# Performance work log

Hardware: AMD Instinct MI355X
Metric: run time of the kernel (lower is better)

## Reference

```python
import jax, jax.numpy as jnp
import numpy as np

N_HEAD = 12
N_TILES = 10  # forward hardcodes t = T // 10 and repeats the tril mask 10x10


def setup_inputs() -> dict:
    key = jax.random.key(0)
    ks = jax.random.split(key, 9)
    B, T, C = 2, 2560, 768
    s = 1.0 / np.sqrt(C)
    x = jax.random.normal(ks[0], (B, T, C), dtype=jnp.float32)
    Wk = jax.random.normal(ks[1], (C, C), dtype=jnp.float32) * s
    bk = jnp.zeros((C,), dtype=jnp.float32)
    Wq = jax.random.normal(ks[2], (C, C), dtype=jnp.float32) * s
    bq = jnp.zeros((C,), dtype=jnp.float32)
    Wv = jax.random.normal(ks[3], (C, C), dtype=jnp.float32) * s
    bv = jnp.zeros((C,), dtype=jnp.float32)
    Wp = jax.random.normal(ks[4], (C, C), dtype=jnp.float32) * s
    bp = jnp.zeros((C,), dtype=jnp.float32)
    return {"x": x, "Wk": Wk, "bk": bk, "Wq": Wq, "bq": bq,
            "Wv": Wv, "bv": bv, "Wp": Wp, "bp": bp}


def reference(x, Wk, bk, Wq, bq, Wv, bv, Wp, bp):
    B, T, C = x.shape
    hd = C // N_HEAD
    t = T // N_TILES
    # linear projections (torch nn.Linear: x @ W.T + b)
    k = (x @ Wk.T + bk).reshape(B, T, N_HEAD, hd).transpose(0, 2, 1, 3)  # [B,H,T,hd]
    q = (x @ Wq.T + bq).reshape(B, T, N_HEAD, hd).transpose(0, 2, 1, 3)
    v = (x @ Wv.T + bv).reshape(B, T, N_HEAD, hd).transpose(0, 2, 1, 3)
    att = jnp.einsum('bhqd,bhkd->bhqk', q, k) * (1.0 / np.sqrt(hd))  # [B,H,T,T]
    # repeated block-tril mask: tril(t,t) tiled 10x10 over TxT
    idx = jnp.arange(T)
    mask = (idx[:, None] % t) >= (idx[None, :] % t)  # [T,T] bool
    att = jnp.where(mask[None, None], att, -jnp.inf)
    att = jax.nn.softmax(att, axis=-1)
    y = jnp.einsum('bhqk,bhkd->bhqd', att, v)  # [B,H,T,hd]
    y = y.transpose(0, 2, 1, 3).reshape(B, T, C)
    return y @ Wp.T + bp
```

## Files before the change

### kernel.cpp

```cpp
#include <hip/hip_runtime.h>

typedef unsigned short u16;
typedef unsigned int u32;
typedef __bf16 bf16x8 __attribute__((ext_vector_type(8)));
typedef short s16x4 __attribute__((ext_vector_type(4)));
typedef float f32x4 __attribute__((ext_vector_type(4)));

#define CC 768
#define TT 2560
#define NH 12
#define HD 64
#define KDIM 768

#define QSCALE 0.18033688011112042f

__device__ __forceinline__ u16 f2bf(float f) {
  u32 u = __builtin_bit_cast(u32, f);
  u32 r = u + 0x7fffu + ((u >> 16) & 1u);
  return (u16)(r >> 16);
}

#if __has_builtin(__builtin_amdgcn_mfma_f32_16x16x16bf16_1k)
__device__ __forceinline__ f32x4 mfma16b(s16x4 a, s16x4 b, f32x4 c) {
  return __builtin_amdgcn_mfma_f32_16x16x16bf16_1k(a, b, c, 0, 0, 0);
}
#else
__device__ __forceinline__ f32x4 mfma16b(s16x4 a, s16x4 b, f32x4 c) {
  f32x4 d;
  asm("v_mfma_f32_16x16x16_bf16 %0, %1, %2, %3\n\ts_nop 7\n\ts_nop 7"
      : "=v"(d) : "v"(a), "v"(b), "v"(c));
  return d;
}
#endif

__global__ void convall(const float* __restrict__ x,
                        const float* __restrict__ Wq, const float* __restrict__ Wk,
                        const float* __restrict__ Wv, const float* __restrict__ Wp,
                        u16* __restrict__ xb, u16* __restrict__ wqb, u16* __restrict__ wkb,
                        u16* __restrict__ wvb, u16* __restrict__ wpb,
                        int nx4, int nw4) {
  int z = blockIdx.y;
  const float* in; u16* out; int n4;
  switch (z) {
    case 0: in = x;  out = xb;  n4 = nx4; break;
    case 1: in = Wq; out = wqb; n4 = nw4; break;
    case 2: in = Wk; out = wkb; n4 = nw4; break;
    case 3: in = Wv; out = wvb; n4 = nw4; break;
    default: in = Wp; out = wpb; n4 = nw4; break;
  }
  int i = blockIdx.x * blockDim.x + threadIdx.x;
  if (i >= n4) return;
  float4 v = ((const float4*)in)[i];
  ushort4 o;
  o.x = f2bf(v.x); o.y = f2bf(v.y); o.z = f2bf(v.z); o.w = f2bf(v.w);
  ((ushort4*)out)[i] = o;
}

__global__ __launch_bounds__(256) void gemm_qkv(
    const u16* __restrict__ xb,
    const u16* __restrict__ wqb, const u16* __restrict__ wkb, const u16* __restrict__ wvb,
    const float* __restrict__ bq, const float* __restrict__ bk, const float* __restrict__ bv,
    u16* __restrict__ qo, u16* __restrict__ ko, u16* __restrict__ vo)
{
  __shared__ __align__(16) u16 lds_a[128 * 72];
  __shared__ __align__(16) u16 lds_b[128 * 72];
  int z = blockIdx.z;
  const u16* W = (z == 0) ? wqb : (z == 1 ? wkb : wvb);
  const float* bias = (z == 0) ? bq : (z == 1 ? bk : bv);
  int n0 = blockIdx.x * 128;
  int m0 = blockIdx.y * 128;
  int tid = threadIdx.x;
  int lane = tid & 63, wv_ = tid >> 6;
  int wm = wv_ & 1, wn = wv_ >> 1;
  int mcol = lane & 15, quad = lane >> 4;
  int chunk = tid & 7, rbase = tid >> 3;

  f32x4 acc[4][4] = {};

  for (int k0 = 0; k0 < KDIM; k0 += 64) {
    __syncthreads();
#pragma unroll
    for (int r = 0; r < 4; ++r) {
      int row = rbase + r * 32;
      *(uint4*)&lds_a[row * 72 + chunk * 8] =
          *(const uint4*)&xb[(size_t)(m0 + row) * KDIM + k0 + chunk * 8];
      *(uint4*)&lds_b[row * 72 + chunk * 8] =
          *(const uint4*)&W[(size_t)(n0 + row) * KDIM + k0 + chunk * 8];
    }
    __syncthreads();
#pragma unroll
    for (int kc = 0; kc < 2; ++kc) {
      bf16x8 af[4], bfr[4];
#pragma unroll
      for (int i = 0; i < 4; i++)
        af[i] = *(const bf16x8*)&lds_a[(wm * 64 + i * 16 + mcol) * 72 + kc * 32 + quad * 8];
#pragma unroll
      for (int i = 0; i < 4; i++)
        bfr[i] = *(const bf16x8*)&lds_b[(wn * 64 + i * 16 + mcol) * 72 + kc * 32 + quad * 8];
      if (z == 2) {
#pragma unroll
        for (int i = 0; i < 4; i++)
#pragma unroll
          for (int j = 0; j < 4; j++)
            acc[i][j] = __builtin_amdgcn_mfma_f32_16x16x32_bf16(af[i], bfr[j], acc[i][j], 0, 0, 0);
      } else {
#pragma unroll
        for (int i = 0; i < 4; i++)
#pragma unroll
          for (int j = 0; j < 4; j++)
            acc[i][j] = __builtin_amdgcn_mfma_f32_16x16x32_bf16(bfr[j], af[i], acc[i][j], 0, 0, 0);
      }
    }
  }

  if (z == 2) {
#pragma unroll
    for (int i = 0; i < 4; i++) {
      int rowb = m0 + wm * 64 + i * 16 + quad * 4;
      int b = rowb / TT;
      int tt0 = rowb - b * TT;
#pragma unroll
      for (int j = 0; j < 4; j++) {
        int col = n0 + wn * 64 + j * 16 + mcol;
        int h = col >> 6, d = col & 63;
        float bb_ = bias[col];
        size_t bhoff = (size_t)(b * NH + h) * (TT * HD);
        ushort4 pk;
        pk.x = f2bf(acc[i][j][0] + bb_);
        pk.y = f2bf(acc[i][j][1] + bb_);
        pk.z = f2bf(acc[i][j][2] + bb_);
        pk.w = f2bf(acc[i][j][3] + bb_);
        *(ushort4*)&vo[bhoff + (size_t)(tt0 >> 4) * 1024 + d * 16 + (tt0 & 15)] = pk;
      }
    }
  } else {
    u16* dst = (z == 0) ? qo : ko;
    float scale = (z == 0) ? QSCALE : 1.0f;
#pragma unroll
    for (int i = 0; i < 4; i++) {
      int token = m0 + wm * 64 + i * 16 + mcol;
      int b = token / TT;
      int tt = token - b * TT;
#pragma unroll
      for (int j = 0; j < 4; j++) {
        int ch0 = n0 + wn * 64 + j * 16 + quad * 4;
        int h = ch0 >> 6, d4 = ch0 & 63;
        float4 bb4 = *(const float4*)&bias[ch0];
        size_t bhoff = (size_t)(b * NH + h) * (TT * HD);
        ushort4 pk;
        pk.x = f2bf((acc[i][j][0] + bb4.x) * scale);
        pk.y = f2bf((acc[i][j][1] + bb4.y) * scale);
        pk.z = f2bf((acc[i][j][2] + bb4.z) * scale);
        pk.w = f2bf((acc[i][j][3] + bb4.w) * scale);
        if (z == 0) {
          *(ushort4*)&dst[bhoff + (size_t)tt * HD + d4] = pk;
        } else {
          *(ushort4*)&dst[bhoff + (size_t)(tt >> 4) * 1024 + (d4 >> 5) * 512 +
                          (tt & 15) * 32 + (d4 & 31)] = pk;
        }
      }
    }
  }
}

struct Strip {
  bf16x8 qf0, qf1;
  f32x4 o0, o1, o2, o3;
  f32x4 racc;
};

__device__ __forceinline__ void strip_step(
    Strip& S, bf16x8 kf0, bf16x8 kf1,
    s16x4 vf0, s16x4 vf1, s16x4 vf2, s16x4 vf3,
    bool maskg, int mcol, int quad)
{
  f32x4 st = {0.f, 0.f, 0.f, 0.f};
  st = __builtin_amdgcn_mfma_f32_16x16x32_bf16(kf0, S.qf0, st, 0, 0, 0);
  st = __builtin_amdgcn_mfma_f32_16x16x32_bf16(kf1, S.qf1, st, 0, 0, 0);
  float p0 = __builtin_amdgcn_exp2f(st[0]);
  float p1 = __builtin_amdgcn_exp2f(st[1]);
  float p2 = __builtin_amdgcn_exp2f(st[2]);
  float p3 = __builtin_amdgcn_exp2f(st[3]);
  if (maskg) {
    int j0 = quad * 4;
    p0 = (j0 + 0 > mcol) ? 0.f : p0;
    p1 = (j0 + 1 > mcol) ? 0.f : p1;
    p2 = (j0 + 2 > mcol) ? 0.f : p2;
    p3 = (j0 + 3 > mcol) ? 0.f : p3;
  }
  uint2 pk;
  pk.x = __builtin_amdgcn_perm(__builtin_bit_cast(u32, p1),
                               __builtin_bit_cast(u32, p0), 0x07060302u);
  pk.y = __builtin_amdgcn_perm(__builtin_bit_cast(u32, p3),
                               __builtin_bit_cast(u32, p2), 0x07060302u);
  s16x4 pf = __builtin_bit_cast(s16x4, pk);
  const s16x4 ones = {0x3F80, 0x3F80, 0x3F80, 0x3F80};
  S.racc = mfma16b(ones, pf, S.racc);
  S.o0 = mfma16b(vf0, pf, S.o0);
  S.o1 = mfma16b(vf1, pf, S.o1);
  S.o2 = mfma16b(vf2, pf, S.o2);
  S.o3 = mfma16b(vf3, pf, S.o3);
}

#define OSTR 68

__global__ __launch_bounds__(128) void attn(
    const u16* __restrict__ q, const u16* __restrict__ kg,
    const u16* __restrict__ vg, u16* __restrict__ y)
{
  __shared__ float lds_o[4][16 * OSTR];
  __shared__ float lds_r[64];

  int tid = threadIdx.x;
  int lane = tid & 63, w = tid >> 6;
  int mcol = lane & 15, quad = lane >> 4;
  int gid = blockIdx.x;
  int c = gid & 7;
  int idx = gid >> 3;
  int sub = idx / 40;
  int s = idx - sub * 40;
  int bh = c * 3 + sub;
  int hb = s >> 3;
  int r = s & 7;
  int b = bh / NH, h = bh - b * NH;
  const u16* qp = q + (size_t)bh * TT * HD;
  const u16* kp = kg + (size_t)bh * TT * HD;
  const u16* vp = vg + (size_t)bh * TT * HD;

  int base = hb * 512;
  int rh = 7 - r;
  int qr[4];
  qr[0] = base + r * 16;
  qr[1] = base + 128 + rh * 16;
  qr[2] = base + 256 + r * 16;
  qr[3] = base + 384 + rh * 16;

  Strip S[4];
#pragma unroll
  for (int i = 0; i < 4; ++i) {
    S[i].qf0 = *(const bf16x8*)&qp[(size_t)(qr[i] + mcol) * HD + quad * 8];
    S[i].qf1 = *(const bf16x8*)&qp[(size_t)(qr[i] + mcol) * HD + 32 + quad * 8];
    S[i].o0 = {0.f, 0.f, 0.f, 0.f};
    S[i].o1 = {0.f, 0.f, 0.f, 0.f};
    S[i].o2 = {0.f, 0.f, 0.f, 0.f};
    S[i].o3 = {0.f, 0.f, 0.f, 0.f};
    S[i].racc = {0.f, 0.f, 0.f, 0.f};
  }

  int koff = mcol * 32 + quad * 8;
  int voff = mcol * 16 + quad * 4;

  for (int kt = w * 10; kt < w * 10 + 10; ++kt) {
    const u16* ktb = kp + kt * (128 * HD);
    const u16* vtb = vp + kt * (128 * HD);
    if ((kt & 1) == 0) {
#pragma unroll
      for (int g = 0; g < 8; ++g) {
        bf16x8 kf0 = *(const bf16x8*)&ktb[g * 1024 + koff];
        bf16x8 kf1 = *(const bf16x8*)&ktb[g * 1024 + 512 + koff];
        s16x4 vf0 = *(const s16x4*)&vtb[g * 1024 + 0 * 256 + voff];
        s16x4 vf1 = *(const s16x4*)&vtb[g * 1024 + 1 * 256 + voff];
        s16x4 vf2 = *(const s16x4*)&vtb[g * 1024 + 2 * 256 + voff];
        s16x4 vf3 = *(const s16x4*)&vtb[g * 1024 + 3 * 256 + voff];
        strip_step(S[1], kf0, kf1, vf0, vf1, vf2, vf3, false, mcol, quad);
        strip_step(S[3], kf0, kf1, vf0, vf1, vf2, vf3, false, mcol, quad);
        if (g <= r) {
          bool mg = (g == r);
          strip_step(S[0], kf0, kf1, vf0, vf1, vf2, vf3, mg, mcol, quad);
          strip_step(S[2], kf0, kf1, vf0, vf1, vf2, vf3, mg, mcol, quad);
        }
      }
    } else {
      for (int g = 0; g <= rh; ++g) {
        bf16x8 kf0 = *(const bf16x8*)&ktb[g * 1024 + koff];
        bf16x8 kf1 = *(const bf16x8*)&ktb[g * 1024 + 512 + koff];
        s16x4 vf0 = *(const s16x4*)&vtb[g * 1024 + 0 * 256 + voff];
        s16x4 vf1 = *(const s16x4*)&vtb[g * 1024 + 1 * 256 + voff];
        s16x4 vf2 = *(const s16x4*)&vtb[g * 1024 + 2 * 256 + voff];
        s16x4 vf3 = *(const s16x4*)&vtb[g * 1024 + 3 * 256 + voff];
        bool mg = (g == rh);
        strip_step(S[1], kf0, kf1, vf0, vf1, vf2, vf3, mg, mcol, quad);
        strip_step(S[3], kf0, kf1, vf0, vf1, vf2, vf3, mg, mcol, quad);
      }
    }
  }

  if (w == 1) {
#pragma unroll
    for (int i = 0; i < 4; ++i) {
      f32x4 oo[4] = {S[i].o0, S[i].o1, S[i].o2, S[i].o3};
#pragma unroll
      for (int df = 0; df < 4; ++df)
        *(f32x4*)&lds_o[i][mcol * OSTR + df * 16 + quad * 4] = oo[df];
      if (quad == 0) lds_r[i * 16 + mcol] = S[i].racc[0];
    }
  }
  __syncthreads();
  if (w == 0) {
#pragma unroll
    for (int i = 0; i < 4; ++i) {
      float denom = S[i].racc[0] + lds_r[i * 16 + mcol];
      float inv = 1.0f / denom;
      f32x4 oo[4] = {S[i].o0, S[i].o1, S[i].o2, S[i].o3};
      size_t yrow = ((size_t)(b * TT + qr[i] + mcol)) * CC + h * HD;
#pragma unroll
      for (int df = 0; df < 4; ++df) {
        f32x4 other = *(const f32x4*)&lds_o[i][mcol * OSTR + df * 16 + quad * 4];
        ushort4 pk;
        pk.x = f2bf((oo[df][0] + other[0]) * inv);
        pk.y = f2bf((oo[df][1] + other[1]) * inv);
        pk.z = f2bf((oo[df][2] + other[2]) * inv);
        pk.w = f2bf((oo[df][3] + other[3]) * inv);
        *(ushort4*)&y[yrow + df * 16 + quad * 4] = pk;
      }
    }
  }
}

__global__ __launch_bounds__(256) void gemm_out(
    const u16* __restrict__ yb, const u16* __restrict__ wpb,
    const float* __restrict__ bp, float* __restrict__ out)
{
  __shared__ __align__(16) u16 lds_a[64 * 72];
  __shared__ __align__(16) u16 lds_b[128 * 72];
  int n0 = blockIdx.x * 128;
  int m0 = blockIdx.y * 64;
  int tid = threadIdx.x;
  int lane = tid & 63, wv_ = tid >> 6;
  int wm = wv_ & 1, wn = wv_ >> 1;
  int mcol = lane & 15, quad = lane >> 4;
  int chunk = tid & 7, rbase = tid >> 3;

  f32x4 acc[2][4] = {};

  for (int k0 = 0; k0 < KDIM; k0 += 64) {
    __syncthreads();
#pragma unroll
    for (int r = 0; r < 2; ++r) {
      int row = rbase + r * 32;
      *(uint4*)&lds_a[row * 72 + chunk * 8] =
          *(const uint4*)&yb[(size_t)(m0 + row) * KDIM + k0 + chunk * 8];
    }
#pragma unroll
    for (int r = 0; r < 4; ++r) {
      int row = rbase + r * 32;
      *(uint4*)&lds_b[row * 72 + chunk * 8] =
          *(const uint4*)&wpb[(size_t)(n0 + row) * KDIM + k0 + chunk * 8];
    }
    __syncthreads();
#pragma unroll
    for (int kc = 0; kc < 2; ++kc) {
      bf16x8 af[2], bfr[4];
#pragma unroll
      for (int i = 0; i < 2; i++)
        af[i] = *(const bf16x8*)&lds_a[(wm * 32 + i * 16 + mcol) * 72 + kc * 32 + quad * 8];
#pragma unroll
      for (int j = 0; j < 4; j++)
        bfr[j] = *(const bf16x8*)&lds_b[(wn * 64 + j * 16 + mcol) * 72 + kc * 32 + quad * 8];
#pragma unroll
      for (int i = 0; i < 2; i++)
#pragma unroll
        for (int j = 0; j < 4; j++)
          acc[i][j] = __builtin_amdgcn_mfma_f32_16x16x32_bf16(bfr[j], af[i], acc[i][j], 0, 0, 0);
    }
  }

#pragma unroll
  for (int i = 0; i < 2; i++) {
    int token = m0 + wm * 32 + i * 16 + mcol;
#pragma unroll
    for (int j = 0; j < 4; j++) {
      int ch0 = n0 + wn * 64 + j * 16 + quad * 4;
      float4 bb4 = *(const float4*)&bp[ch0];
      float4 o4;
      o4.x = acc[i][j][0] + bb4.x;
      o4.y = acc[i][j][1] + bb4.y;
      o4.z = acc[i][j][2] + bb4.z;
      o4.w = acc[i][j][3] + bb4.w;
      *(float4*)&out[(size_t)token * CC + ch0] = o4;
    }
  }
}

extern "C" void kernel_launch(void* const* d_in, const int* in_sizes, int n_in,
                              void* d_out, int out_size, void* d_ws, size_t ws_size,
                              hipStream_t stream) {
  const float* x  = (const float*)d_in[0];
  const float* Wk = (const float*)d_in[1];
  const float* bk = (const float*)d_in[2];
  const float* Wq = (const float*)d_in[3];
  const float* bq = (const float*)d_in[4];
  const float* Wv = (const float*)d_in[5];
  const float* bv = (const float*)d_in[6];
  const float* Wp = (const float*)d_in[7];
  const float* bp = (const float*)d_in[8];
  float* out = (float*)d_out;

  char* ws = (char*)d_ws;
  size_t off = 0;
  auto alloc = [&](size_t bytes) {
    void* p = ws + off;
    off += (bytes + 255) & ~(size_t)255;
    return p;
  };
  const size_t NX = (size_t)2 * TT * CC;
  const size_t NW = (size_t)CC * CC;
  u16* xb  = (u16*)alloc(NX * 2);
  u16* wqb = (u16*)alloc(NW * 2);
  u16* wkb = (u16*)alloc(NW * 2);
  u16* wvb = (u16*)alloc(NW * 2);
  u16* wpb = (u16*)alloc(NW * 2);
  u16* qws = (u16*)alloc(NX * 2);
  u16* kws = (u16*)alloc(NX * 2);
  u16* vgw = (u16*)alloc(NX * 2);
  u16* yws = (u16*)alloc(NX * 2);

  int nx4 = (int)(NX / 4), nw4 = (int)(NW / 4);
  convall<<<dim3((nx4 + 255) / 256, 5), 256, 0, stream>>>(
      x, Wq, Wk, Wv, Wp, xb, wqb, wkb, wvb, wpb, nx4, nw4);

  gemm_qkv<<<dim3(6, 40, 3), 256, 0, stream>>>(xb, wqb, wkb, wvb, bq, bk, bv,
                                               qws, kws, vgw);
  attn<<<dim3(960), 128, 0, stream>>>(qws, kws, vgw, yws);
  gemm_out<<<dim3(6, 80), 256, 0, stream>>>(yws, wpb, bp, out);
}
```

Before: 188.8 us.

## Fuse Q/K/V projections into one block sharing the x tile

The QKV GEMM no longer runs a separate grid slice per projection. Each block now computes a 64x64 output tile for all three of Q, K and V at once, loading the x tile into LDS once and reusing it against three weight tiles. This cuts redundant x loads and raises the block count from 720 to 960. In exchange each block does less MFMA work per LDS fragment load, because the per-wave tiles shrink to 32x32 per matrix, and more weight traffic is issued per block.

```diff
diff --git a/kernel.cpp b/kernel.cpp
--- a/kernel.cpp
+++ b/kernel.cpp
@@ -62,103 +62,107 @@
     const float* __restrict__ bq, const float* __restrict__ bk, const float* __restrict__ bv,
     u16* __restrict__ qo, u16* __restrict__ ko, u16* __restrict__ vo)
 {
-  __shared__ __align__(16) u16 lds_a[128 * 72];
-  __shared__ __align__(16) u16 lds_b[128 * 72];
-  int z = blockIdx.z;
-  const u16* W = (z == 0) ? wqb : (z == 1 ? wkb : wvb);
-  const float* bias = (z == 0) ? bq : (z == 1 ? bk : bv);
-  int n0 = blockIdx.x * 128;
-  int m0 = blockIdx.y * 128;
+  __shared__ __align__(16) u16 lds_a[64 * 72];
+  __shared__ __align__(16) u16 lds_b[3][64 * 72];
+  int n0 = blockIdx.x * 64;
+  int m0 = blockIdx.y * 64;
   int tid = threadIdx.x;
   int lane = tid & 63, wv_ = tid >> 6;
   int wm = wv_ & 1, wn = wv_ >> 1;
   int mcol = lane & 15, quad = lane >> 4;
   int chunk = tid & 7, rbase = tid >> 3;
 
-  f32x4 acc[4][4] = {};
+  const u16* Ws0 = wqb; const u16* Ws1 = wkb; const u16* Ws2 = wvb;
+
+  f32x4 acc[3][2][2] = {};
 
   for (int k0 = 0; k0 < KDIM; k0 += 64) {
     __syncthreads();
 #pragma unroll
-    for (int r = 0; r < 4; ++r) {
+    for (int r = 0; r < 2; ++r) {
       int row = rbase + r * 32;
       *(uint4*)&lds_a[row * 72 + chunk * 8] =
           *(const uint4*)&xb[(size_t)(m0 + row) * KDIM + k0 + chunk * 8];
-      *(uint4*)&lds_b[row * 72 + chunk * 8] =
-          *(const uint4*)&W[(size_t)(n0 + row) * KDIM + k0 + chunk * 8];
+      *(uint4*)&lds_b[0][row * 72 + chunk * 8] =
+          *(const uint4*)&Ws0[(size_t)(n0 + row) * KDIM + k0 + chunk * 8];
+      *(uint4*)&lds_b[1][row * 72 + chunk * 8] =
+          *(const uint4*)&Ws1[(size_t)(n0 + row) * KDIM + k0 + chunk * 8];
+      *(uint4*)&lds_b[2][row * 72 + chunk * 8] =
+          *(const uint4*)&Ws2[(size_t)(n0 + row) * KDIM + k0 + chunk * 8];
     }
     __syncthreads();
 #pragma unroll
     for (int kc = 0; kc < 2; ++kc) {
-      bf16x8 af[4], bfr[4];
-#pragma unroll
-      for (int i = 0; i < 4; i++)
-        af[i] = *(const bf16x8*)&lds_a[(wm * 64 + i * 16 + mcol) * 72 + kc * 32 + quad * 8];
-#pragma unroll
-      for (int i = 0; i < 4; i++)
-        bfr[i] = *(const bf16x8*)&lds_b[(wn * 64 + i * 16 + mcol) * 72 + kc * 32 + quad * 8];
-      if (z == 2) {
-#pragma unroll
-        for (int i = 0; i < 4; i++)
-#pragma unroll
-          for (int j = 0; j < 4; j++)
-            acc[i][j] = __builtin_amdgcn_mfma_f32_16x16x32_bf16(af[i], bfr[j], acc[i][j], 0, 0, 0);
-      } else {
-#pragma unroll
-        for (int i = 0; i < 4; i++)
-#pragma unroll
-          for (int j = 0; j < 4; j++)
-            acc[i][j] = __builtin_amdgcn_mfma_f32_16x16x32_bf16(bfr[j], af[i], acc[i][j], 0, 0, 0);
-      }
-    }
-  }
-
-  if (z == 2) {
-#pragma unroll
-    for (int i = 0; i < 4; i++) {
-      int rowb = m0 + wm * 64 + i * 16 + quad * 4;
-      int b = rowb / TT;
-      int tt0 = rowb - b * TT;
-#pragma unroll
-      for (int j = 0; j < 4; j++) {
-        int col = n0 + wn * 64 + j * 16 + mcol;
-        int h = col >> 6, d = col & 63;
-        float bb_ = bias[col];
-        size_t bhoff = (size_t)(b * NH + h) * (TT * HD);
-        ushort4 pk;
-        pk.x = f2bf(acc[i][j][0] + bb_);
-        pk.y = f2bf(acc[i][j][1] + bb_);
-        pk.z = f2bf(acc[i][j][2] + bb_);
-        pk.w = f2bf(acc[i][j][3] + bb_);
-        *(ushort4*)&vo[bhoff + (size_t)(tt0 >> 4) * 1024 + d * 16 + (tt0 & 15)] = pk;
-      }
-    }
-  } else {
-    u16* dst = (z == 0) ? qo : ko;
-    float scale = (z == 0) ? QSCALE : 1.0f;
-#pragma unroll
-    for (int i = 0; i < 4; i++) {
-      int token = m0 + wm * 64 + i * 16 + mcol;
-      int b = token / TT;
-      int tt = token - b * TT;
-#pragma unroll
-      for (int j = 0; j < 4; j++) {
-        int ch0 = n0 + wn * 64 + j * 16 + quad * 4;
-        int h = ch0 >> 6, d4 = ch0 & 63;
-        float4 bb4 = *(const float4*)&bias[ch0];
-        size_t bhoff = (size_t)(b * NH + h) * (TT * HD);
-        ushort4 pk;
-        pk.x = f2bf((acc[i][j][0] + bb4.x) * scale);
-        pk.y = f2bf((acc[i][j][1] + bb4.y) * scale);
-        pk.z = f2bf((acc[i][j][2] + bb4.z) * scale);
-        pk.w = f2bf((acc[i][j][3] + bb4.w) * scale);
-        if (z == 0) {
-          *(ushort4*)&dst[bhoff + (size_t)tt * HD + d4] = pk;
+      bf16x8 af[2];
+#pragma unroll
+      for (int i = 0; i < 2; i++)
+        af[i] = *(const bf16x8*)&lds_a[(wm * 32 + i * 16 + mcol) * 72 + kc * 32 + quad * 8];
+#pragma unroll
+      for (int z = 0; z < 3; ++z) {
+        bf16x8 bfr[2];
+#pragma unroll
+        for (int j = 0; j < 2; j++)
+          bfr[j] = *(const bf16x8*)&lds_b[z][(wn * 32 + j * 16 + mcol) * 72 + kc * 32 + quad * 8];
+        if (z == 2) {
+#pragma unroll
+          for (int i = 0; i < 2; i++)
+#pragma unroll
+            for (int j = 0; j < 2; j++)
+              acc[z][i][j] = __builtin_amdgcn_mfma_f32_16x16x32_bf16(af[i], bfr[j], acc[z][i][j], 0, 0, 0);
         } else {
-          *(ushort4*)&dst[bhoff + (size_t)(tt >> 4) * 1024 + (d4 >> 5) * 512 +
-                          (tt & 15) * 32 + (d4 & 31)] = pk;
+#pragma unroll
+          for (int i = 0; i < 2; i++)
+#pragma unroll
+            for (int j = 0; j < 2; j++)
+              acc[z][i][j] = __builtin_amdgcn_mfma_f32_16x16x32_bf16(bfr[j], af[i], acc[z][i][j], 0, 0, 0);
         }
       }
+    }
+  }
+
+#pragma unroll
+  for (int i = 0; i < 2; i++) {
+    int token = m0 + wm * 32 + i * 16 + mcol;
+    int b = token / TT;
+    int tt = token - b * TT;
+#pragma unroll
+    for (int j = 0; j < 2; j++) {
+      int ch0 = n0 + wn * 32 + j * 16 + quad * 4;
+      int h = ch0 >> 6, d4 = ch0 & 63;
+      size_t bhoff = (size_t)(b * NH + h) * (TT * HD);
+      float4 bq4 = *(const float4*)&bq[ch0];
+      float4 bk4 = *(const float4*)&bk[ch0];
+      ushort4 pq, pk_;
+      pq.x = f2bf((acc[0][i][j][0] + bq4.x) * QSCALE);
+      pq.y = f2bf((acc[0][i][j][1] + bq4.y) * QSCALE);
+      pq.z = f2bf((acc[0][i][j][2] + bq4.z) * QSCALE);
+      pq.w = f2bf((acc[0][i][j][3] + bq4.w) * QSCALE);
+      *(ushort4*)&qo[bhoff + (size_t)tt * HD + d4] = pq;
+      pk_.x = f2bf(acc[1][i][j][0] + bk4.x);
+      pk_.y = f2bf(acc[1][i][j][1] + bk4.y);
+      pk_.z = f2bf(acc[1][i][j][2] + bk4.z);
+      pk_.w = f2bf(acc[1][i][j][3] + bk4.w);
+      *(ushort4*)&ko[bhoff + (size_t)(tt >> 4) * 1024 + (d4 >> 5) * 512 +
+                     (tt & 15) * 32 + (d4 & 31)] = pk_;
+    }
+  }
+#pragma unroll
+  for (int i = 0; i < 2; i++) {
+    int rowb = m0 + wm * 32 + i * 16 + quad * 4;
+    int b = rowb / TT;
+    int tt0 = rowb - b * TT;
+#pragma unroll
+    for (int j = 0; j < 2; j++) {
+      int col = n0 + wn * 32 + j * 16 + mcol;
+      int h = col >> 6, d = col & 63;
+      float bb_ = bv[col];
+      size_t bhoff = (size_t)(b * NH + h) * (TT * HD);
+      ushort4 pk;
+      pk.x = f2bf(acc[2][i][j][0] + bb_);
+      pk.y = f2bf(acc[2][i][j][1] + bb_);
+      pk.z = f2bf(acc[2][i][j][2] + bb_);
+      pk.w = f2bf(acc[2][i][j][3] + bb_);
+      *(ushort4*)&vo[bhoff + (size_t)(tt0 >> 4) * 1024 + d * 16 + (tt0 & 15)] = pk;
     }
   }
 }
@@ -419,8 +423,8 @@
   convall<<<dim3((nx4 + 255) / 256, 5), 256, 0, stream>>>(
       x, Wq, Wk, Wv, Wp, xb, wqb, wkb, wvb, wpb, nx4, nw4);
 
-  gemm_qkv<<<dim3(6, 40, 3), 256, 0, stream>>>(xb, wqb, wkb, wvb, bq, bk, bv,
-                                               qws, kws, vgw);
+  gemm_qkv<<<dim3(12, 80), 256, 0, stream>>>(xb, wqb, wkb, wvb, bq, bk, bv,
+                                             qws, kws, vgw);
   attn<<<dim3(960), 128, 0, stream>>>(qws, kws, vgw, yws);
   gemm_out<<<dim3(6, 80), 256, 0, stream>>>(yws, wpb, bp, out);
 }
```

New measurement: 223.0 us. 1.18x slower.
